# Performance work log

Measured on AMD Instinct MI355X. Metric: run time of the kernel, lower is better.

The kernel has to match this reference:

```python
import jax, jax.numpy as jnp
import numpy as np

B, D, H, O, E = 16384, 1024, 512, 256, 8


def setup_inputs() -> dict:
    key = jax.random.key(0)
    ks = jax.random.split(key, 8)
    s = lambda k, shape, fan: (jax.random.normal(k, shape, jnp.float32) / np.sqrt(fan).astype(np.float32))
    z = lambda shape: jnp.zeros(shape, jnp.float32)
    return {
        "x": jax.random.normal(ks[0], (B, D), jnp.float32),
        # gating network: D -> 256 -> 128 -> E
        "gw1": s(ks[1], (D, 256), D), "gb1": z((256,)),
        "gw2": s(ks[2], (256, 128), 256), "gb2": z((128,)),
        "gw3": s(ks[3], (128, E), 128), "gb3": z((E,)),
        # experts, batched over expert dim E: D -> H -> H -> O
        "ew1": s(ks[4], (E, D, H), D), "eb1": z((E, H)),
        "ew2": s(ks[5], (E, H, H), H), "eb2": z((E, H)),
        "ew3": s(ks[6], (E, H, O), H), "eb3": z((E, O)),
    }


def reference(x, gw1, gb1, gw2, gb2, gw3, gb3, ew1, eb1, ew2, eb2, ew3, eb3):
    # Gating network (dropout is identity in eval mode)
    g = jax.nn.relu(x @ gw1 + gb1)
    g = jax.nn.relu(g @ gw2 + gb2)
    gates = jax.nn.softmax(g @ gw3 + gb3, axis=1)  # [B, E]
    # All experts run on every token: batched small MLPs over expert axis e
    h = jax.nn.relu(jnp.einsum('bd,edh->ebh', x, ew1) + eb1[:, None, :])   # [E, B, H]
    h = jax.nn.relu(jnp.einsum('ebh,ehk->ebk', h, ew2) + eb2[:, None, :])  # [E, B, H]
    eo = jnp.einsum('ebh,eho->ebo', h, ew3) + eb3[:, None, :]              # [E, B, O]
    # gate-weighted sum over experts
    out = jnp.einsum('ebo,be->bo', eo, gates)  # [B, O]
    return out
```

## Files before the change

### kernel.cpp

```cpp
#include <hip/hip_runtime.h>
#include <hip/hip_bf16.h>

typedef __hip_bfloat16 bf16;
typedef __attribute__((ext_vector_type(8))) __bf16 bf16x8;
typedef __attribute__((ext_vector_type(4))) float f32x4;

#define B_ 16384
#define D_ 1024
#define H_ 512
#define O_ 256
#define E_ 8
#define BC_ 4096

#define GLDS(src, dst) __builtin_amdgcn_global_load_lds( \
    (const __attribute__((address_space(1))) void*)(src), \
    (__attribute__((address_space(3))) void*)(dst), 16, 0, 0)

__global__ void detect_k(const unsigned short* __restrict__ x, int* __restrict__ flag) {
    __shared__ int s;
    if (threadIdx.x == 0) s = 0;
    __syncthreads();
    int big = 0;
    for (int i = threadIdx.x; i < 2048; i += 256)
        if (((x[i] >> 7) & 0xFF) >= 150) big = 1;
    if (big) atomicOr(&s, 1);
    __syncthreads();
    if (threadIdx.x == 0) *flag = s;
}

__global__ void cvt_k(const void* __restrict__ src, bf16* __restrict__ dst,
                      const int* __restrict__ flag, long n) {
    const int f = *flag;
    long i = (long)blockIdx.x * blockDim.x + threadIdx.x;
    const long stride = (long)gridDim.x * blockDim.x;
    if (f) {
        const float* s = (const float*)src;
        for (; i < n; i += stride) dst[i] = __float2bfloat16(s[i]);
    } else {
        const bf16* s = (const bf16*)src;
        for (; i < n; i += stride) dst[i] = s[i];
    }
}

__global__ void transpose_k(const void* __restrict__ in, bf16* __restrict__ out,
                            const int* __restrict__ flag, int R, int C) {
    __shared__ bf16 t[32][33];
    const int f = *flag;
    const long zo = (long)blockIdx.z * R * C;
    const int x = blockIdx.x * 32 + threadIdx.x;
    const int y0 = blockIdx.y * 32;
    const float* inf = (const float*)in;
    const bf16* inb = (const bf16*)in;
#pragma unroll
    for (int i = 0; i < 4; i++) {
        int r = y0 + threadIdx.y + i * 8;
        long idx = zo + (long)r * C + x;
        t[threadIdx.y + i * 8][threadIdx.x] =
            f ? __float2bfloat16(inf[idx]) : inb[idx];
    }
    __syncthreads();
    const int xr = blockIdx.y * 32 + threadIdx.x;
#pragma unroll
    for (int i = 0; i < 4; i++) {
        int c = blockIdx.x * 32 + threadIdx.y + i * 8;
        out[zo + (long)c * R + xr] = t[threadIdx.x][threadIdx.y + i * 8];
    }
}

__global__ void gate3_softmax_k(const bf16* __restrict__ g2,
                                const bf16* __restrict__ gw3,
                                const bf16* __restrict__ gb3,
                                float* __restrict__ gates) {
    __shared__ float w[128 * 8];
    __shared__ float bsh[8];
    const int tid = threadIdx.x;
    for (int i = tid; i < 1024; i += 256) w[i] = __bfloat162float(gw3[i]);
    if (tid < 8) bsh[tid] = __bfloat162float(gb3[tid]);
    __syncthreads();

    const long row = (long)blockIdx.x * 256 + tid;
    float acc[8];
#pragma unroll
    for (int o = 0; o < 8; o++) acc[o] = bsh[o];

    const bf16x8* rp8 = (const bf16x8*)(g2 + row * 128);
#pragma unroll 4
    for (int c8 = 0; c8 < 16; c8++) {
        bf16x8 v8 = rp8[c8];
#pragma unroll
        for (int jj = 0; jj < 8; jj++) {
            float v = (float)v8[jj];
            int k = c8 * 8 + jj;
#pragma unroll
            for (int o = 0; o < 8; o++) acc[o] += v * w[k * 8 + o];
        }
    }
    float m = acc[0];
#pragma unroll
    for (int o = 1; o < 8; o++) m = fmaxf(m, acc[o]);
    float s = 0.f;
#pragma unroll
    for (int o = 0; o < 8; o++) { acc[o] = __expf(acc[o] - m); s += acc[o]; }
    const float inv = 1.f / s;
#pragma unroll
    for (int o = 0; o < 8; o++) gates[row * 8 + o] = acc[o] * inv;
}

template <int MODE>
__global__ __launch_bounds__(256, 2)
void gemm_bt(const bf16* __restrict__ A, const bf16* __restrict__ Bt,
             const bf16* __restrict__ bias, const float* __restrict__ gates,
             void* __restrict__ Cout, const bf16* __restrict__ eb3,
             const int* __restrict__ oflag,
             int lda, int ldb, int ldo, int K,
             long a_z, long b_z, long bias_z, long out_z,
             int e_gate, int k_per_e, long a_e, long b_e, long row0) {
    __shared__ __attribute__((aligned(16))) bf16 As[128 * 32];
    __shared__ __attribute__((aligned(16))) bf16 Bs[128 * 32];

    const int tid  = threadIdx.x;
    const int lane = tid & 63;
    const int quad = lane >> 4;
    const int l15  = lane & 15;
    const int wid  = tid >> 6;
    const int wr   = (wid >> 1) << 6;
    const int wc   = (wid & 1) << 6;
    const int z    = blockIdx.z;
    const long m0  = (long)blockIdx.y << 7;
    const long n0  = (long)blockIdx.x << 7;

    const bf16* Az = A + (long)z * a_z;
    const bf16* Bz = Bt + (long)z * b_z;

    f32x4 acc[4][4];
#pragma unroll
    for (int i = 0; i < 4; i++)
#pragma unroll
        for (int j = 0; j < 4; j++) acc[i][j] = (f32x4){0.f, 0.f, 0.f, 0.f};

    const int erow = tid >> 2;
    const int ecol = (tid & 3) << 3;

    const int n_e   = k_per_e ? (K / k_per_e) : 1;
    const int inner = (k_per_e ? k_per_e : K) >> 5;

    for (int e = 0; e < n_e; e++) {
        const bf16* Ae = Az + (long)e * a_e;
        const bf16* Be = Bz + (long)e * b_e;
        for (int kti = 0; kti < inner; kti++) {
            const int kk = kti << 5;
#pragma unroll
            for (int i = 0; i < 2; i++) {
                const int r = (i << 6) + erow;
                GLDS(Ae + (m0 + r) * lda + (kk + ecol), As + r * 32 + ecol);
            }
#pragma unroll
            for (int i = 0; i < 2; i++) {
                const int r = (i << 6) + erow;
                GLDS(Be + (n0 + r) * ldb + (kk + ecol), Bs + r * 32 + ecol);
            }
            __syncthreads();
            bf16x8 af[4], bfr[4];
#pragma unroll
            for (int i = 0; i < 4; i++)
                af[i] = *(const bf16x8*)(As + (wr + i * 16 + l15) * 32 + (quad << 3));
#pragma unroll
            for (int j = 0; j < 4; j++)
                bfr[j] = *(const bf16x8*)(Bs + (wc + j * 16 + l15) * 32 + (quad << 3));
#pragma unroll
            for (int i = 0; i < 4; i++)
#pragma unroll
                for (int j = 0; j < 4; j++)
                    acc[i][j] = __builtin_amdgcn_mfma_f32_16x16x32_bf16(
                        af[i], bfr[j], acc[i][j], 0, 0, 0);
            __syncthreads();
        }
    }

    const int eg = (e_gate >= 0) ? e_gate : z;

    if constexpr (MODE == 0 || MODE == 1) {
        bf16* C = (bf16*)Cout + (long)z * out_z;
        const bf16* bb = bias + (long)z * bias_z;
        float gv[4][4];
        if constexpr (MODE == 1) {
#pragma unroll
            for (int i = 0; i < 4; i++)
#pragma unroll
                for (int rg = 0; rg < 4; rg++)
                    gv[i][rg] = gates[(row0 + m0 + wr + i * 16 + quad * 4 + rg) * 8 + eg];
        }
#pragma unroll
        for (int j = 0; j < 4; j++) {
            const int c = (int)n0 + wc + j * 16 + l15;
            const float bv = __bfloat162float(bb[c]);
#pragma unroll
            for (int i = 0; i < 4; i++) {
#pragma unroll
                for (int rg = 0; rg < 4; rg++) {
                    const long r = m0 + wr + i * 16 + quad * 4 + rg;
                    float v = fmaxf(acc[i][j][rg] + bv, 0.f);
                    if constexpr (MODE == 1) v *= gv[i][rg];
                    C[r * ldo + c] = __float2bfloat16(v);
                }
            }
        }
    } else if constexpr (MODE == 2) {
        float* C = (float*)Cout;
#pragma unroll
        for (int i = 0; i < 4; i++) {
#pragma unroll
            for (int rg = 0; rg < 4; rg++) {
                const long r = m0 + wr + i * 16 + quad * 4 + rg;
                const float g = gates[(row0 + r) * 8 + eg];
#pragma unroll
                for (int j = 0; j < 4; j++) {
                    const int c = (int)n0 + wc + j * 16 + l15;
                    const float b3 = __bfloat162float(eb3[eg * O_ + c]);
                    C[r * ldo + c] += acc[i][j][rg] + g * b3;
                }
            }
        }
    } else {
        const int f = *oflag;
        float b3[4][8];
#pragma unroll
        for (int j = 0; j < 4; j++) {
            const int c = (int)n0 + wc + j * 16 + l15;
#pragma unroll
            for (int e = 0; e < 8; e++)
                b3[j][e] = __bfloat162float(eb3[e * O_ + c]);
        }
#pragma unroll
        for (int i = 0; i < 4; i++) {
#pragma unroll
            for (int rg = 0; rg < 4; rg++) {
                const long r = m0 + wr + i * 16 + quad * 4 + rg;
                const float* gp = gates + (row0 + r) * 8;
#pragma unroll
                for (int j = 0; j < 4; j++) {
                    const int c = (int)n0 + wc + j * 16 + l15;
                    float v = acc[i][j][rg];
#pragma unroll
                    for (int e = 0; e < 8; e++) v += gp[e] * b3[j][e];
                    if (f) ((float*)Cout)[(row0 + r) * ldo + c] = v;
                    else   ((bf16*)Cout)[(row0 + r) * ldo + c] = __float2bfloat16(v);
                }
            }
        }
    }
}

__global__ void zero_f32_k(float* __restrict__ p) {
    p[(long)blockIdx.x * 256 + threadIdx.x] = 0.f;
}
__global__ void out_cvt_k(const float* __restrict__ in, void* __restrict__ out,
                          const int* __restrict__ flag) {
    const long i = (long)blockIdx.x * 256 + threadIdx.x;
    if (*flag) ((float*)out)[i] = in[i];
    else       ((bf16*)out)[i] = __float2bfloat16(in[i]);
}

extern "C" void kernel_launch(void* const* d_in, const int* in_sizes, int n_in,
                              void* d_out, int out_size, void* d_ws, size_t ws_size,
                              hipStream_t stream) {
    (void)in_sizes; (void)n_in; (void)out_size;
    const void* x   = d_in[0];
    const void* gw1 = d_in[1];
    const void* gb1 = d_in[2];
    const void* gw2 = d_in[3];
    const void* gb2 = d_in[4];
    const void* gw3 = d_in[5];
    const void* gb3 = d_in[6];
    const void* ew1 = d_in[7];
    const void* eb1 = d_in[8];
    const void* ew2 = d_in[9];
    const void* eb2 = d_in[10];
    const void* ew3 = d_in[11];
    const void* eb3 = d_in[12];

    char* ws = (char*)d_ws;
    size_t off = 0;
    auto alloc = [&](size_t n) { char* p = ws + off; off += (n + 255) & ~(size_t)255; return p; };

    int*  flag  = (int*)alloc(256);
    bf16* xc    = (bf16*)alloc((size_t)B_ * D_ * 2);
    bf16* gw1t  = (bf16*)alloc((size_t)256 * 1024 * 2);
    bf16* gw2t  = (bf16*)alloc((size_t)128 * 256 * 2);
    bf16* ew1t  = (bf16*)alloc((size_t)E_ * H_ * D_ * 2);
    bf16* ew2t  = (bf16*)alloc((size_t)E_ * H_ * H_ * 2);
    bf16* ew3t  = (bf16*)alloc((size_t)E_ * O_ * H_ * 2);
    bf16* gb1c  = (bf16*)alloc(256 * 2);
    bf16* gb2c  = (bf16*)alloc(128 * 2);
    bf16* gw3c  = (bf16*)alloc(1024 * 2);
    bf16* gb3c  = (bf16*)alloc(8 * 2);
    bf16* eb1c  = (bf16*)alloc((size_t)E_ * H_ * 2);
    bf16* eb2c  = (bf16*)alloc((size_t)E_ * H_ * 2);
    bf16* eb3c  = (bf16*)alloc((size_t)E_ * O_ * 2);
    bf16* g1    = (bf16*)alloc((size_t)B_ * 256 * 2);
    bf16* g2b   = (bf16*)alloc((size_t)B_ * 128 * 2);
    float* gates = (float*)alloc((size_t)B_ * 8 * 4);

    const size_t small = off;
    const size_t needA = small + ((size_t)E_ * BC_ * H_ * 2 + 256)
                               + ((size_t)E_ * B_ * H_ * 2 + 256) + 4096;
    const bool pathA = ws_size >= needA;

    detect_k<<<1, 256, 0, stream>>>((const unsigned short*)x, flag);

    cvt_k<<<4096, 256, 0, stream>>>(x, xc, flag, (long)B_ * D_);
    cvt_k<<<1, 256, 0, stream>>>(gb1, gb1c, flag, 256);
    cvt_k<<<1, 256, 0, stream>>>(gb2, gb2c, flag, 128);
    cvt_k<<<4, 256, 0, stream>>>(gw3, gw3c, flag, 1024);
    cvt_k<<<1, 256, 0, stream>>>(gb3, gb3c, flag, 8);
    cvt_k<<<16, 256, 0, stream>>>(eb1, eb1c, flag, (long)E_ * H_);
    cvt_k<<<16, 256, 0, stream>>>(eb2, eb2c, flag, (long)E_ * H_);
    cvt_k<<<8, 256, 0, stream>>>(eb3, eb3c, flag, (long)E_ * O_);

    transpose_k<<<dim3(256 / 32, 1024 / 32, 1), dim3(32, 8), 0, stream>>>(gw1, gw1t, flag, 1024, 256);
    transpose_k<<<dim3(128 / 32, 256 / 32, 1), dim3(32, 8), 0, stream>>>(gw2, gw2t, flag, 256, 128);
    transpose_k<<<dim3(H_ / 32, D_ / 32, E_), dim3(32, 8), 0, stream>>>(ew1, ew1t, flag, D_, H_);
    transpose_k<<<dim3(H_ / 32, H_ / 32, E_), dim3(32, 8), 0, stream>>>(ew2, ew2t, flag, H_, H_);
    transpose_k<<<dim3(O_ / 32, H_ / 32, E_), dim3(32, 8), 0, stream>>>(ew3, ew3t, flag, H_, O_);

    gemm_bt<0><<<dim3(2, 128, 1), 256, 0, stream>>>(
        xc, gw1t, gb1c, nullptr, g1, nullptr, nullptr,
        1024, 1024, 256, 1024, 0, 0, 0, 0, 0, 0, 0, 0, 0);
    gemm_bt<0><<<dim3(1, 128, 1), 256, 0, stream>>>(
        g1, gw2t, gb2c, nullptr, g2b, nullptr, nullptr,
        256, 256, 128, 256, 0, 0, 0, 0, 0, 0, 0, 0, 0);
    gate3_softmax_k<<<dim3(B_ / 256), 256, 0, stream>>>(g2b, gw3c, gb3c, gates);

    if (pathA) {
        bf16* h1 = (bf16*)alloc((size_t)E_ * BC_ * H_ * 2);
        bf16* h2 = (bf16*)alloc((size_t)E_ * B_ * H_ * 2);
        for (int ci = 0; ci < B_ / BC_; ci++) {
            const long rb = (long)ci * BC_;
            gemm_bt<0><<<dim3(4, BC_ / 128, 8), 256, 0, stream>>>(
                xc + rb * D_, ew1t, eb1c, nullptr, h1, nullptr, nullptr,
                D_, D_, H_, D_,
                0, (long)H_ * D_, H_, (long)BC_ * H_, 0, 0, 0, 0, 0);
            gemm_bt<1><<<dim3(4, BC_ / 128, 8), 256, 0, stream>>>(
                h1, ew2t, eb2c, gates, h2 + rb * H_, nullptr, nullptr,
                H_, H_, H_, H_,
                (long)BC_ * H_, (long)H_ * H_, H_, (long)B_ * H_, -1, 0, 0, 0, rb);
        }
        gemm_bt<3><<<dim3(2, B_ / 128, 1), 256, 0, stream>>>(
            h2, ew3t, nullptr, gates, d_out, eb3c, flag,
            H_, H_, O_, E_ * H_,
            0, 0, 0, 0, 0, H_, (long)B_ * H_, (long)O_ * H_, 0);
    } else {
        bf16* h1s = (bf16*)alloc((size_t)B_ * H_ * 2);
        bf16* h2s = (bf16*)alloc((size_t)B_ * H_ * 2);
        float* oacc = (float*)alloc((size_t)B_ * O_ * 4);
        zero_f32_k<<<dim3(B_ * O_ / 256), 256, 0, stream>>>(oacc);
        for (int e = 0; e < E_; e++) {
            gemm_bt<0><<<dim3(4, 128, 1), 256, 0, stream>>>(
                xc, ew1t + (size_t)e * H_ * D_, eb1c + (size_t)e * H_, nullptr, h1s, nullptr, nullptr,
                1024, 1024, 512, 1024, 0, 0, 0, 0, 0, 0, 0, 0, 0);
            gemm_bt<1><<<dim3(4, 128, 1), 256, 0, stream>>>(
                h1s, ew2t + (size_t)e * H_ * H_, eb2c + (size_t)e * H_, gates, h2s, nullptr, nullptr,
                512, 512, 512, 512, 0, 0, 0, 0, e, 0, 0, 0, 0);
            gemm_bt<2><<<dim3(2, 128, 1), 256, 0, stream>>>(
                h2s, ew3t + (size_t)e * O_ * H_, nullptr, gates, oacc, eb3c, nullptr,
                512, 512, 256, 512, 0, 0, 0, 0, e, 0, 0, 0, 0);
        }
        out_cvt_k<<<dim3(B_ * O_ / 256), 256, 0, stream>>>(oacc, d_out, flag);
    }
}
```

Baseline: 604.0 us.

## Fuse final expert GEMM into the chunk loop with split-K atomic accumulation

The third expert GEMM now runs inside each row chunk, so the second layer's activations stay in a per-chunk buffer instead of a full-batch one across all experts. The final GEMM is split over four expert pairs along the grid z dimension. Each split atomically adds its gate-weighted partial result into a zeroed fp32 accumulator, which a separate kernel then converts to the output dtype. The chunk size is doubled, which cuts the number of launches and the intermediate traffic. In exchange it adds fp32 atomic contention, an extra zero pass and an extra conversion pass over the output.

New measurement: 669.6 us. 1.11x slower.

```diff
diff --git a/kernel.cpp b/kernel.cpp
--- a/kernel.cpp
+++ b/kernel.cpp
@@ -10,7 +10,7 @@
 #define H_ 512
 #define O_ 256
 #define E_ 8
-#define BC_ 4096
+#define BC_ 8192
 
 #define GLDS(src, dst) __builtin_amdgcn_global_load_lds( \
     (const __attribute__((address_space(1))) void*)(src), \
@@ -222,29 +222,28 @@
             }
         }
     } else {
-        const int f = *oflag;
+        float* C = (float*)Cout;
+        const int epz = e_gate;
+        const int e0  = z * epz;
         float b3[4][8];
 #pragma unroll
         for (int j = 0; j < 4; j++) {
             const int c = (int)n0 + wc + j * 16 + l15;
-#pragma unroll
-            for (int e = 0; e < 8; e++)
-                b3[j][e] = __bfloat162float(eb3[e * O_ + c]);
+            for (int s = 0; s < epz; s++)
+                b3[j][s] = __bfloat162float(eb3[(e0 + s) * O_ + c]);
         }
 #pragma unroll
         for (int i = 0; i < 4; i++) {
 #pragma unroll
             for (int rg = 0; rg < 4; rg++) {
                 const long r = m0 + wr + i * 16 + quad * 4 + rg;
-                const float* gp = gates + (row0 + r) * 8;
+                const float* gp = gates + (row0 + r) * 8 + e0;
 #pragma unroll
                 for (int j = 0; j < 4; j++) {
                     const int c = (int)n0 + wc + j * 16 + l15;
                     float v = acc[i][j][rg];
-#pragma unroll
-                    for (int e = 0; e < 8; e++) v += gp[e] * b3[j][e];
-                    if (f) ((float*)Cout)[(row0 + r) * ldo + c] = v;
-                    else   ((bf16*)Cout)[(row0 + r) * ldo + c] = __float2bfloat16(v);
+                    for (int s = 0; s < epz; s++) v += gp[s] * b3[j][s];
+                    atomicAdd(C + (row0 + r) * ldo + c, v);
                 }
             }
         }
@@ -302,8 +301,8 @@
     float* gates = (float*)alloc((size_t)B_ * 8 * 4);
 
     const size_t small = off;
-    const size_t needA = small + ((size_t)E_ * BC_ * H_ * 2 + 256)
-                               + ((size_t)E_ * B_ * H_ * 2 + 256) + 4096;
+    const size_t needA = small + 2ull * ((size_t)E_ * BC_ * H_ * 2 + 256)
+                               + ((size_t)B_ * O_ * 4 + 256) + 4096;
     const bool pathA = ws_size >= needA;
 
     detect_k<<<1, 256, 0, stream>>>((const unsigned short*)x, flag);
@@ -332,23 +331,27 @@
     gate3_softmax_k<<<dim3(B_ / 256), 256, 0, stream>>>(g2b, gw3c, gb3c, gates);
 
     if (pathA) {
-        bf16* h1 = (bf16*)alloc((size_t)E_ * BC_ * H_ * 2);
-        bf16* h2 = (bf16*)alloc((size_t)E_ * B_ * H_ * 2);
+        bf16* h1c = (bf16*)alloc((size_t)E_ * BC_ * H_ * 2);
+        bf16* h2c = (bf16*)alloc((size_t)E_ * BC_ * H_ * 2);
+        float* oacc = (float*)alloc((size_t)B_ * O_ * 4);
+        zero_f32_k<<<dim3(B_ * O_ / 256), 256, 0, stream>>>(oacc);
         for (int ci = 0; ci < B_ / BC_; ci++) {
             const long rb = (long)ci * BC_;
             gemm_bt<0><<<dim3(4, BC_ / 128, 8), 256, 0, stream>>>(
-                xc + rb * D_, ew1t, eb1c, nullptr, h1, nullptr, nullptr,
+                xc + rb * D_, ew1t, eb1c, nullptr, h1c, nullptr, nullptr,
                 D_, D_, H_, D_,
                 0, (long)H_ * D_, H_, (long)BC_ * H_, 0, 0, 0, 0, 0);
             gemm_bt<1><<<dim3(4, BC_ / 128, 8), 256, 0, stream>>>(
-                h1, ew2t, eb2c, gates, h2 + rb * H_, nullptr, nullptr,
+                h1c, ew2t, eb2c, gates, h2c, nullptr, nullptr,
                 H_, H_, H_, H_,
-                (long)BC_ * H_, (long)H_ * H_, H_, (long)B_ * H_, -1, 0, 0, 0, rb);
-        }
-        gemm_bt<3><<<dim3(2, B_ / 128, 1), 256, 0, stream>>>(
-            h2, ew3t, nullptr, gates, d_out, eb3c, flag,
-            H_, H_, O_, E_ * H_,
-            0, 0, 0, 0, 0, H_, (long)B_ * H_, (long)O_ * H_, 0);
+                (long)BC_ * H_, (long)H_ * H_, H_, (long)BC_ * H_, -1, 0, 0, 0, rb);
+            gemm_bt<4><<<dim3(2, BC_ / 128, 4), 256, 0, stream>>>(
+                h2c, ew3t, nullptr, gates, oacc, eb3c, nullptr,
+                H_, H_, O_, 1024,
+                2L * BC_ * H_, 2L * O_ * H_, 0, 0,
+                2 , 512, (long)BC_ * H_, (long)O_ * H_, rb);
+        }
+        out_cvt_k<<<dim3(B_ * O_ / 256), 256, 0, stream>>>(oacc, d_out, flag);
     } else {
         bf16* h1s = (bf16*)alloc((size_t)B_ * H_ * 2);
         bf16* h2s = (bf16*)alloc((size_t)B_ * H_ * 2);
```
